# Performance work log

Measured on AMD Instinct MI355X. Metric: run time of the kernel, lower is better.

The kernel has to match this reference:

```python
import jax, jax.numpy as jnp
import numpy as np

B, ID, OD = 4096, 2048, 1024


def _conv_softmax(x, w):
    # x: [..., L]; torch Conv1d(1,1,k=3,stride=1,pad=1,bias=False) then softmax(dim=-1)
    L = x.shape[-1]
    xp = jnp.pad(x, [(0, 0)] * (x.ndim - 1) + [(1, 1)])
    y = w[0] * xp[..., 0:L] + w[1] * xp[..., 1:L + 1] + w[2] * xp[..., 2:L + 2]
    return jax.nn.softmax(y, axis=-1)


def _lstm_cell(x, h, c, Wih, Whh, bih, bhh):
    # torch LSTMCell gate order: i, f, g, o
    g = x @ Wih.T + h @ Whh.T + (bih + bhh)
    i, f, gg, o = jnp.split(g, 4, axis=-1)
    c2 = jax.nn.sigmoid(f) * c + jax.nn.sigmoid(i) * jnp.tanh(gg)
    h2 = jax.nn.sigmoid(o) * jnp.tanh(c2)
    return h2, c2


def _lstm_params(key, in_dim, hid):
    k = 1.0 / np.sqrt(hid)
    ks = jax.random.split(key, 4)
    Wih = jax.random.uniform(ks[0], (4 * hid, in_dim), jnp.float32, -k, k)
    Whh = jax.random.uniform(ks[1], (4 * hid, hid), jnp.float32, -k, k)
    bih = jax.random.uniform(ks[2], (4 * hid,), jnp.float32, -k, k)
    bhh = jax.random.uniform(ks[3], (4 * hid,), jnp.float32, -k, k)
    return Wih, Whh, bih, bhh


def setup_inputs() -> dict:
    key = jax.random.key(0)
    ks = jax.random.split(key, 12)
    spec = jax.random.normal(ks[0], (B, ID), jnp.float32)
    Wih1, Whh1, bih1, bhh1 = _lstm_params(ks[1], ID, OD)
    Wih2, Whh2, bih2, bhh2 = _lstm_params(ks[2], ID // 2, OD // 2)
    Wih3, Whh3, bih3, bhh3 = _lstm_params(ks[3], ID // 4, OD // 4)
    Wih4, Whh4, bih4, bhh4 = _lstm_params(ks[4], ID // 8, OD // 8)
    ck = np.sqrt(1.0 / 3.0)  # Conv1d(1,1,3) init bound
    w2_1h = jax.random.uniform(ks[5], (3,), jnp.float32, -ck, ck)
    w2_1c = jax.random.uniform(ks[6], (3,), jnp.float32, -ck, ck)
    w3_2h = jax.random.uniform(ks[7], (3,), jnp.float32, -ck, ck)
    w3_2c = jax.random.uniform(ks[8], (3,), jnp.float32, -ck, ck)
    w4_3h = jax.random.uniform(ks[9], (3,), jnp.float32, -ck, ck)
    w4_3c = jax.random.uniform(ks[10], (3,), jnp.float32, -ck, ck)
    return dict(spec=spec,
                Wih1=Wih1, Whh1=Whh1, bih1=bih1, bhh1=bhh1,
                Wih2=Wih2, Whh2=Whh2, bih2=bih2, bhh2=bhh2,
                Wih3=Wih3, Whh3=Whh3, bih3=bih3, bhh3=bhh3,
                Wih4=Wih4, Whh4=Whh4, bih4=bih4, bhh4=bhh4,
                w2_1h=w2_1h, w2_1c=w2_1c, w3_2h=w3_2h, w3_2c=w3_2c,
                w4_3h=w4_3h, w4_3c=w4_3c)


def reference(spec, Wih1, Whh1, bih1, bhh1, Wih2, Whh2, bih2, bhh2,
              Wih3, Whh3, bih3, bhh3, Wih4, Whh4, bih4, bhh4,
              w2_1h, w2_1c, w3_2h, w3_2c, w4_3h, w4_3c):
    b = spec.shape[0]
    # Level 4: 8 independent steps, fresh zero state each (torch code passes no hidden)
    x4 = spec.reshape(b, 8, ID // 8)
    z4 = jnp.zeros((b, 8, OD // 8), spec.dtype)
    h4, c4 = _lstm_cell(x4, z4, z4, Wih4, Whh4, bih4, bhh4)   # [b,8,OD/8]
    hb4 = _conv_softmax(h4.reshape(b, 4, OD // 4), w4_3h)      # pairs -> [b,4,OD/4]
    cb4 = _conv_softmax(c4.reshape(b, 4, OD // 4), w4_3c)
    # Level 3: 4 independent steps seeded by level-4 blended states
    x3 = spec.reshape(b, 4, ID // 4)
    h3, c3 = _lstm_cell(x3, hb4, cb4, Wih3, Whh3, bih3, bhh3)  # [b,4,OD/4]
    hb3 = _conv_softmax(h3.reshape(b, 2, OD // 2), w3_2h)      # [b,2,OD/2]
    cb3 = _conv_softmax(c3.reshape(b, 2, OD // 2), w3_2c)
    # Level 2: 2 independent steps
    x2 = spec.reshape(b, 2, ID // 2)
    h2, c2 = _lstm_cell(x2, hb3, cb3, Wih2, Whh2, bih2, bhh2)  # [b,2,OD/2]
    hb2 = _conv_softmax(h2.reshape(b, OD), w2_1h)              # [b,OD]
    cb2 = _conv_softmax(c2.reshape(b, OD), w2_1c)
    # Level 1: single full-resolution step; forward returns out1 = h1
    h1, c1 = _lstm_cell(spec, hb2, cb2, Wih1, Whh1, bih1, bhh1)
    return h1
```

## Files before the change

kernel.cpp:

```cpp
#include <hip/hip_runtime.h>


typedef __bf16 bf16x8 __attribute__((ext_vector_type(8)));
typedef float f32x4 __attribute__((ext_vector_type(4)));
typedef unsigned short u16x4 __attribute__((ext_vector_type(4)));
typedef unsigned short u16x8 __attribute__((ext_vector_type(8)));

#define AS1 __attribute__((address_space(1)))
#define AS3 __attribute__((address_space(3)))

__device__ __forceinline__ unsigned short f2bf(float f) {
    union { float f; unsigned int i; } v; v.f = f;
    unsigned int r = v.i + 0x7fffu + ((v.i >> 16) & 1u);
    return (unsigned short)(r >> 16);
}
__device__ __forceinline__ float bf2f(unsigned short u) {
    union { unsigned int i; float f; } v; v.i = ((unsigned int)u) << 16; return v.f;
}
__device__ __forceinline__ float sigm(float x) { return 1.f / (1.f + __expf(-x)); }
__device__ __forceinline__ float tanh_(float x) { float e = __expf(2.f * x); return 1.f - 2.f / (e + 1.f); }

struct PSeg { const float* src; unsigned short* dst; long g0; int H; int kshift; int dstld; int dstcol; };
struct PArgs {
    PSeg s[7];
    const float* spec; unsigned short* sB;
    const float *bi1, *bh1, *bi2, *bh2, *bi3, *bh3, *bi4, *bh4;
    float *bs1, *bs2, *bs3, *bs4;
};

__global__ __launch_bounds__(256) void prep_all(PArgs pa)
{
    const long NS = 2097152;
    const long NP = 4161536;
    const long total = NS + NP + 7680;
    const long stride = (long)gridDim.x * blockDim.x;
    for (long gi = (long)blockIdx.x * blockDim.x + threadIdx.x; gi < total; gi += stride) {
        if (gi < NS) {
            const float4 v = ((const float4*)pa.spec)[gi];
            u16x4 o; o.x = f2bf(v.x); o.y = f2bf(v.y); o.z = f2bf(v.z); o.w = f2bf(v.w);
            ((u16x4*)pa.sB)[gi] = o;
        } else if (gi < NS + NP) {
            const long gp = gi - NS;
            int si = 0;
#pragma unroll
            for (int k = 1; k < 7; ++k) si += (gp >= pa.s[k].g0);
            const PSeg sg = pa.s[si];
            const long i = gp - sg.g0;
            const int kq = 1 << sg.kshift;
            const int p = (int)(i >> sg.kshift);
            const int kk = ((int)i & (kq - 1)) << 2;
            const int o = ((p >> 6) << 4) | (p & 15);
            const int q = (p >> 4) & 3;
            const long r = (long)q * sg.H + o;
            const float4 v = *(const float4*)(sg.src + (r << (sg.kshift + 2)) + kk);
            u16x4 wv; wv.x = f2bf(v.x); wv.y = f2bf(v.y); wv.z = f2bf(v.z); wv.w = f2bf(v.w);
            *(u16x4*)(sg.dst + (long)p * sg.dstld + sg.dstcol + kk) = wv;
        } else {
            const int i = (int)(gi - NS - NP);
            const float *bih, *bhh; float* dst; int H, j;
            if (i < 4096)      { bih = pa.bi1; bhh = pa.bh1; dst = pa.bs1; H = 1024; j = i; }
            else if (i < 6144) { bih = pa.bi2; bhh = pa.bh2; dst = pa.bs2; H = 512;  j = i - 4096; }
            else if (i < 7168) { bih = pa.bi3; bhh = pa.bh3; dst = pa.bs3; H = 256;  j = i - 6144; }
            else               { bih = pa.bi4; bhh = pa.bh4; dst = pa.bs4; H = 128;  j = i - 7168; }
            const int o = ((j >> 6) << 4) | (j & 15);
            const int q = (j >> 4) & 3;
            dst[j] = bih[q * H + o] + bhh[q * H + o];
        }
    }
}

#define GLL(gsrc, loff) __builtin_amdgcn_global_load_lds(                                   \
    (const AS1 void*)(gsrc), (AS3 void*)(lds + (loff)), 16, 0, 0)

#define FENCE asm volatile("" ::: "memory")

#define STAGE_A(tts, qq)                                                                    \
    { if ((tts) < nk0) {                                                                    \
        const size_t ko = (size_t)(tts) * 64;                                               \
        GLL(A0 + a0off + ko,                   ((qq) << 15) + sd);                          \
        GLL(A0 + a0off + (size_t)32*K0 + ko,   ((qq) << 15) + 4096 + sd);                   \
        GLL(A0 + a0off + (size_t)64*K0 + ko,   ((qq) << 15) + 8192 + sd);                   \
        GLL(A0 + a0off + (size_t)96*K0 + ko,   ((qq) << 15) + 12288 + sd);                  \
    } else {                                                                                \
        const size_t ko = (size_t)((tts) - nk0) * 64;                                       \
        GLL(A1 + a1off + ko,                   ((qq) << 15) + sd);                          \
        GLL(A1 + a1off + (size_t)32*K1 + ko,   ((qq) << 15) + 4096 + sd);                   \
        GLL(A1 + a1off + (size_t)64*K1 + ko,   ((qq) << 15) + 8192 + sd);                   \
        GLL(A1 + a1off + (size_t)96*K1 + ko,   ((qq) << 15) + 12288 + sd);                  \
    } }

#define STAGE_B(tts, qq)                                                                    \
    { const size_t ko = (size_t)(tts) * 64;                                                 \
        GLL(W + boff + ko,                   ((qq) << 15) + 16384 + sd);                    \
        GLL(W + boff + (size_t)32*K + ko,    ((qq) << 15) + 20480 + sd);                    \
        GLL(W + boff + (size_t)64*K + ko,    ((qq) << 15) + 24576 + sd);                    \
        GLL(W + boff + (size_t)96*K + ko,    ((qq) << 15) + 28672 + sd); }

#define CLUSTER(MI, AF)                                                                     \
    { _Pragma("unroll") for (int mi = 0; mi < 2; ++mi) {                                    \
        _Pragma("unroll") for (int ni = 0; ni < 2; ++ni) {                                  \
            acc[(MI)+mi][ni] = __builtin_amdgcn_mfma_f32_16x16x32_bf16(                     \
                AF[mi][0], bF0[ni][0], acc[(MI)+mi][ni], 0, 0, 0);                          \
            acc[(MI)+mi][ni] = __builtin_amdgcn_mfma_f32_16x16x32_bf16(                     \
                AF[mi][1], bF0[ni][1], acc[(MI)+mi][ni], 0, 0, 0);                          \
            acc[(MI)+mi][ni+2] = __builtin_amdgcn_mfma_f32_16x16x32_bf16(                   \
                AF[mi][0], bF1[ni][0], acc[(MI)+mi][ni+2], 0, 0, 0);                        \
            acc[(MI)+mi][ni+2] = __builtin_amdgcn_mfma_f32_16x16x32_bf16(                   \
                AF[mi][1], bF1[ni][1], acc[(MI)+mi][ni+2], 0, 0, 0);                        \
    } } }

template<bool HAS_CIN, bool LAST>
__global__ __launch_bounds__(256, 2) void gemm8(
    const unsigned short* __restrict__ A0, const unsigned short* __restrict__ A1,
    const int K0, const int K1,
    const unsigned short* __restrict__ W,
    const float* __restrict__ bsum, const unsigned short* __restrict__ Cin,
    float* __restrict__ HoutF, unsigned short* __restrict__ HoutB,
    unsigned short* __restrict__ CoutB, const int H)
{
    __shared__ __align__(16) char lds[65536];
    const int t = threadIdx.x;
    const int w = t >> 6, l = t & 63;
    const int wr = w >> 1, wc = w & 1;
    const int K = K0 + K1;
    const int nk0 = K0 >> 6;

    const int GX = gridDim.x, GY = gridDim.y;
    const int nwg = GX * GY;
    const int bid = (int)blockIdx.y * GX + (int)blockIdx.x;
    const int swz = (bid & 7) * (nwg >> 3) + (bid >> 3);
    const int m0 = (swz / GY) * 128, n0 = (swz % GY) * 128;

    const int colsw = ((t & 7) ^ ((t >> 3) & 7)) * 8;
    const size_t a0off = (size_t)(m0 + (t >> 3)) * K0 + colsw;
    const size_t a1off = (size_t)(m0 + (t >> 3)) * K1 + colsw;
    const size_t boff  = (size_t)(n0 + (t >> 3)) * K  + colsw;
    const int sd = t * 16;

    const int lr128 = (l & 15) * 128;
    const int sw0 = (((l >> 4)    ) ^ (l & 7)) * 16;
    const int sw1 = (((l >> 4) + 4) ^ (l & 7)) * 16;

    f32x4 acc[4][4];
#pragma unroll
    for (int i = 0; i < 4; ++i)
#pragma unroll
        for (int j = 0; j < 4; ++j) acc[i][j] = (f32x4){0.f, 0.f, 0.f, 0.f};

    const int NT = K >> 6;

    STAGE_A(0, 0);
    STAGE_B(0, 0);
    STAGE_B(1, 1);

    bf16x8 aLo[2][2], aHi[2][2], bF0[2][2], bF1[2][2];

    for (int tt = 0; tt < NT; ++tt) {
        const int q = tt & 1, qn = q ^ 1;
        const int rbA = (q << 15) + wr * 8192 + lr128;
        const int rbB = (q << 15) + 16384 + wc * 8192 + lr128;
        const bool st1 = (tt + 1 < NT), st2 = (tt + 2 < NT);

        if (st1) { asm volatile("s_waitcnt vmcnt(4)" ::: "memory"); }
        else     { asm volatile("s_waitcnt vmcnt(0)" ::: "memory"); }
        __builtin_amdgcn_s_barrier();
        FENCE;

#pragma unroll
        for (int mi = 0; mi < 2; ++mi) {
            aLo[mi][0] = *(const bf16x8*)(lds + rbA + mi * 2048 + sw0);
            aLo[mi][1] = *(const bf16x8*)(lds + rbA + mi * 2048 + sw1);
        }
#pragma unroll
        for (int ni = 0; ni < 2; ++ni) {
            bF0[ni][0] = *(const bf16x8*)(lds + rbB + ni * 2048 + sw0);
            bF0[ni][1] = *(const bf16x8*)(lds + rbB + ni * 2048 + sw1);
            bF1[ni][0] = *(const bf16x8*)(lds + rbB + 4096 + ni * 2048 + sw0);
            bF1[ni][1] = *(const bf16x8*)(lds + rbB + 4096 + ni * 2048 + sw1);
        }
        if (st1) { STAGE_A(tt + 1, qn); }
#pragma unroll
        for (int mi = 0; mi < 2; ++mi) {
            aHi[mi][0] = *(const bf16x8*)(lds + rbA + 4096 + mi * 2048 + sw0);
            aHi[mi][1] = *(const bf16x8*)(lds + rbA + 4096 + mi * 2048 + sw1);
        }

        __builtin_amdgcn_s_setprio(1);
        CLUSTER(0, aLo);
        __builtin_amdgcn_s_setprio(0);
        __builtin_amdgcn_s_barrier();
        FENCE;

        if (st2) { STAGE_B(tt + 2, q); }
        __builtin_amdgcn_s_setprio(1);
        CLUSTER(2, aHi);
        __builtin_amdgcn_s_setprio(0);
    }

    const int ocol = (n0 >> 6) * 16 + wc * 16 + (l & 15);
    const int bb = n0 + wc * 64 + (l & 15);
    const float b0 = bsum[bb], b1 = bsum[bb + 16], b2 = bsum[bb + 32], b3 = bsum[bb + 48];
    const int mrow0 = m0 + wr * 64 + (l >> 4) * 4;
#pragma unroll
    for (int mi = 0; mi < 4; ++mi)
#pragma unroll
        for (int j = 0; j < 4; ++j) {
            const size_t m = (size_t)(mrow0 + mi * 16 + j);
            const float gi = acc[mi][0][j] + b0;
            const float gf = acc[mi][1][j] + b1;
            const float gg = acc[mi][2][j] + b2;
            const float go = acc[mi][3][j] + b3;
            float c2 = sigm(gi) * tanh_(gg);
            if (HAS_CIN) c2 += sigm(gf) * bf2f(Cin[m * H + ocol]);
            const float h2 = sigm(go) * tanh_(c2);
            if (LAST) {
                HoutF[m * H + ocol] = h2;
            } else {
                HoutB[m * H + ocol] = f2bf(h2);
                CoutB[m * H + ocol] = f2bf(c2);
            }
        }
}

template<int L>
__global__ __launch_bounds__(256) void conv_dual(
    const unsigned short* __restrict__ Hin, const unsigned short* __restrict__ Cin,
    const float* __restrict__ w3h, const float* __restrict__ w3c,
    unsigned short* __restrict__ hbuf, unsigned short* __restrict__ cbuf)
{
    constexpr int R = 2048 / L;
    constexpr int TPR = L / 8;
    __shared__ float xs[R][L + 2];
    __shared__ float red[8];
    const int nb = gridDim.x >> 1;
    const bool isC = (int)blockIdx.x >= nb;
    const int row0 = (isC ? (int)blockIdx.x - nb : (int)blockIdx.x) * R;
    const unsigned short* Xs = isC ? Cin : Hin;
    const float* w3 = isC ? w3c : w3h;
    const int t = threadIdx.x;
    const int r = t / TPR;
    const int c8 = (t % TPR) * 8;
    const float w0 = w3[0], w1 = w3[1], w2 = w3[2];

    const u16x8 v = *(const u16x8*)(Xs + (size_t)(row0 + r) * L + c8);
#pragma unroll
    for (int k = 0; k < 8; ++k) xs[r][c8 + 1 + k] = bf2f(v[k]);
    if (t < R) { xs[t][0] = 0.f; xs[t][L + 1] = 0.f; }
    __syncthreads();

    float y[8];
    float vmax = -3.4e38f;
#pragma unroll
    for (int k = 0; k < 8; ++k) {
        y[k] = w0 * xs[r][c8 + k] + w1 * xs[r][c8 + k + 1] + w2 * xs[r][c8 + k + 2];
        vmax = fmaxf(vmax, y[k]);
    }
#pragma unroll
    for (int off = (TPR >= 64 ? 32 : TPR / 2); off >= 1; off >>= 1)
        vmax = fmaxf(vmax, __shfl_xor(vmax, off));
    if (TPR == 128) {
        if ((t & 63) == 0) red[t >> 6] = vmax;
        __syncthreads();
        vmax = fmaxf(red[2 * r], red[2 * r + 1]);
    }
    float s = 0.f;
#pragma unroll
    for (int k = 0; k < 8; ++k) { y[k] = __expf(y[k] - vmax); s += y[k]; }
#pragma unroll
    for (int off = (TPR >= 64 ? 32 : TPR / 2); off >= 1; off >>= 1)
        s += __shfl_xor(s, off);
    if (TPR == 128) {
        if ((t & 63) == 0) red[4 + (t >> 6)] = s;
        __syncthreads();
        s = red[4 + 2 * r] + red[4 + 2 * r + 1];
    }
    const float inv = 1.f / s;
    u16x8 o;
#pragma unroll
    for (int k = 0; k < 8; ++k) o[k] = f2bf(y[k] * inv);
    if (isC) *(u16x8*)(cbuf + (size_t)(row0 + r) * L + c8) = o;
    else     *(u16x8*)(hbuf + (size_t)(row0 + r) * L + c8) = o;
}

extern "C" void kernel_launch(void* const* d_in, const int* in_sizes, int n_in,
                              void* d_out, int out_size, void* d_ws, size_t ws_size,
                              hipStream_t stream)
{
    (void)in_sizes; (void)n_in; (void)out_size; (void)ws_size;
    const float* spec  = (const float*)d_in[0];
    const float* Wih1  = (const float*)d_in[1];
    const float* Whh1  = (const float*)d_in[2];
    const float* bih1  = (const float*)d_in[3];
    const float* bhh1  = (const float*)d_in[4];
    const float* Wih2  = (const float*)d_in[5];
    const float* Whh2  = (const float*)d_in[6];
    const float* bih2  = (const float*)d_in[7];
    const float* bhh2  = (const float*)d_in[8];
    const float* Wih3  = (const float*)d_in[9];
    const float* Whh3  = (const float*)d_in[10];
    const float* bih3  = (const float*)d_in[11];
    const float* bhh3  = (const float*)d_in[12];
    const float* Wih4  = (const float*)d_in[13];
    const float* bih4  = (const float*)d_in[15];
    const float* bhh4  = (const float*)d_in[16];
    const float* w2_1h = (const float*)d_in[17];
    const float* w2_1c = (const float*)d_in[18];
    const float* w3_2h = (const float*)d_in[19];
    const float* w3_2c = (const float*)d_in[20];
    const float* w4_3h = (const float*)d_in[21];
    const float* w4_3c = (const float*)d_in[22];

    char* ws = (char*)d_ws;
    unsigned short* h   = (unsigned short*)(ws + 0);
    unsigned short* c   = (unsigned short*)(ws + (size_t)8388608);
    unsigned short* cb  = (unsigned short*)(ws + (size_t)16777216);
    unsigned short* hb  = (unsigned short*)(ws + (size_t)25165824);
    unsigned short* sB  = (unsigned short*)(ws + (size_t)33554432);
    unsigned short* Wc1 = (unsigned short*)(ws + (size_t)50331648);
    unsigned short* Wc2 = (unsigned short*)(ws + (size_t)75497472);
    unsigned short* Wc3 = (unsigned short*)(ws + (size_t)81788928);
    unsigned short* W4  = (unsigned short*)(ws + (size_t)83361792);
    float*          bs1 = (float*)(ws + (size_t)83623936);
    float*          bs2 = bs1 + 4096;
    float*          bs3 = bs2 + 4096;
    float*          bs4 = bs3 + 4096;

    PArgs pa;
    pa.s[0] = { Wih1, Wc1,       0, 1024, 9, 3072,    0 };
    pa.s[1] = { Whh1, Wc1, 2097152, 1024, 8, 3072, 2048 };
    pa.s[2] = { Wih2, Wc2, 3145728,  512, 8, 1536,    0 };
    pa.s[3] = { Whh2, Wc2, 3670016,  512, 7, 1536, 1024 };
    pa.s[4] = { Wih3, Wc3, 3932160,  256, 7,  768,    0 };
    pa.s[5] = { Whh3, Wc3, 4063232,  256, 6,  768,  512 };
    pa.s[6] = { Wih4, W4,  4128768,  128, 6,  256,    0 };
    pa.spec = spec; pa.sB = sB;
    pa.bi1 = bih1; pa.bh1 = bhh1; pa.bi2 = bih2; pa.bh2 = bhh2;
    pa.bi3 = bih3; pa.bh3 = bhh3; pa.bi4 = bih4; pa.bh4 = bhh4;
    pa.bs1 = bs1; pa.bs2 = bs2; pa.bs3 = bs3; pa.bs4 = bs4;
    prep_all<<<2048, 256, 0, stream>>>(pa);

    gemm8<false, false><<<dim3(256, 4), 256, 0, stream>>>(
        sB, nullptr, 256, 0, W4, bs4, nullptr, nullptr, h, c, 128);
    conv_dual<256><<<4096, 256, 0, stream>>>(h, c, w4_3h, w4_3c, hb, cb);

    gemm8<true, false><<<dim3(128, 8), 256, 0, stream>>>(
        sB, hb, 512, 256, Wc3, bs3, cb, nullptr, h, c, 256);
    conv_dual<512><<<4096, 256, 0, stream>>>(h, c, w3_2h, w3_2c, hb, cb);

    gemm8<true, false><<<dim3(64, 16), 256, 0, stream>>>(
        sB, hb, 1024, 512, Wc2, bs2, cb, nullptr, h, c, 512);
    conv_dual<1024><<<4096, 256, 0, stream>>>(h, c, w2_1h, w2_1c, hb, cb);

    gemm8<true, true><<<dim3(32, 32), 256, 0, stream>>>(
        sB, hb, 2048, 1024, Wc1, bs1, cb, (float*)d_out, nullptr, nullptr, 1024);
}
```

Before: 301.6 us.

## Enlarge GEMM workgroup tile to 256x256 with 16 waves

The fused LSTM-gate GEMM kernel moves from 128x128 tiles with 4 waves to 256x256 tiles with 16 waves per workgroup, arranged as a 4x4 wave grid. The LDS double buffer grows to 128KB and each thread now issues two global-to-LDS loads per operand per stage instead of four. Grids shrink by 4x, so the largest GEMM launches 256 workgroups instead of 1024. The aim is more operand reuse per global load and less redundant traffic, at the cost of one workgroup per CU, heavier barrier synchronisation, and reduced latency hiding.

New measurement: 522.8 us. 1.73x slower.

```diff
diff --git a/kernel.cpp b/kernel.cpp
--- a/kernel.cpp
+++ b/kernel.cpp
@@ -77,24 +77,18 @@
 #define STAGE_A(tts, qq)                                                                    \
     { if ((tts) < nk0) {                                                                    \
         const size_t ko = (size_t)(tts) * 64;                                               \
-        GLL(A0 + a0off + ko,                   ((qq) << 15) + sd);                          \
-        GLL(A0 + a0off + (size_t)32*K0 + ko,   ((qq) << 15) + 4096 + sd);                   \
-        GLL(A0 + a0off + (size_t)64*K0 + ko,   ((qq) << 15) + 8192 + sd);                   \
-        GLL(A0 + a0off + (size_t)96*K0 + ko,   ((qq) << 15) + 12288 + sd);                  \
+        GLL(A0 + a0off0 + ko, ((qq) << 16) + sd);                                           \
+        GLL(A0 + a0off1 + ko, ((qq) << 16) + 16384 + sd);                                   \
     } else {                                                                                \
         const size_t ko = (size_t)((tts) - nk0) * 64;                                       \
-        GLL(A1 + a1off + ko,                   ((qq) << 15) + sd);                          \
-        GLL(A1 + a1off + (size_t)32*K1 + ko,   ((qq) << 15) + 4096 + sd);                   \
-        GLL(A1 + a1off + (size_t)64*K1 + ko,   ((qq) << 15) + 8192 + sd);                   \
-        GLL(A1 + a1off + (size_t)96*K1 + ko,   ((qq) << 15) + 12288 + sd);                  \
+        GLL(A1 + a1off0 + ko, ((qq) << 16) + sd);                                           \
+        GLL(A1 + a1off1 + ko, ((qq) << 16) + 16384 + sd);                                   \
     } }
 
 #define STAGE_B(tts, qq)                                                                    \
     { const size_t ko = (size_t)(tts) * 64;                                                 \
-        GLL(W + boff + ko,                   ((qq) << 15) + 16384 + sd);                    \
-        GLL(W + boff + (size_t)32*K + ko,    ((qq) << 15) + 20480 + sd);                    \
-        GLL(W + boff + (size_t)64*K + ko,    ((qq) << 15) + 24576 + sd);                    \
-        GLL(W + boff + (size_t)96*K + ko,    ((qq) << 15) + 28672 + sd); }
+        GLL(W + boff0 + ko, ((qq) << 16) + 32768 + sd);                                     \
+        GLL(W + boff1 + ko, ((qq) << 16) + 49152 + sd); }
 
 #define CLUSTER(MI, AF)                                                                     \
     { _Pragma("unroll") for (int mi = 0; mi < 2; ++mi) {                                    \
@@ -110,7 +104,7 @@
     } } }
 
 template<bool HAS_CIN, bool LAST>
-__global__ __launch_bounds__(256, 2) void gemm8(
+__global__ __launch_bounds__(1024, 1) void gemm16(
     const unsigned short* __restrict__ A0, const unsigned short* __restrict__ A1,
     const int K0, const int K1,
     const unsigned short* __restrict__ W,
@@ -118,10 +112,10 @@
     float* __restrict__ HoutF, unsigned short* __restrict__ HoutB,
     unsigned short* __restrict__ CoutB, const int H)
 {
-    __shared__ __align__(16) char lds[65536];
+    __shared__ __align__(16) char lds[131072];
     const int t = threadIdx.x;
     const int w = t >> 6, l = t & 63;
-    const int wr = w >> 1, wc = w & 1;
+    const int wr = w >> 2, wc = w & 3;
     const int K = K0 + K1;
     const int nk0 = K0 >> 6;
 
@@ -129,12 +123,16 @@
     const int nwg = GX * GY;
     const int bid = (int)blockIdx.y * GX + (int)blockIdx.x;
     const int swz = (bid & 7) * (nwg >> 3) + (bid >> 3);
-    const int m0 = (swz / GY) * 128, n0 = (swz % GY) * 128;
+    const int m0 = (swz / GY) * 256, n0 = (swz % GY) * 256;
 
     const int colsw = ((t & 7) ^ ((t >> 3) & 7)) * 8;
-    const size_t a0off = (size_t)(m0 + (t >> 3)) * K0 + colsw;
-    const size_t a1off = (size_t)(m0 + (t >> 3)) * K1 + colsw;
-    const size_t boff  = (size_t)(n0 + (t >> 3)) * K  + colsw;
+    const int arow = m0 + (t >> 3);
+    const size_t a0off0 = (size_t)arow * K0 + colsw;
+    const size_t a0off1 = a0off0 + (size_t)128 * K0;
+    const size_t a1off0 = (size_t)arow * K1 + colsw;
+    const size_t a1off1 = a1off0 + (size_t)128 * K1;
+    const size_t boff0 = (size_t)(n0 + (t >> 3)) * K + colsw;
+    const size_t boff1 = boff0 + (size_t)128 * K;
     const int sd = t * 16;
 
     const int lr128 = (l & 15) * 128;
@@ -157,11 +155,11 @@
 
     for (int tt = 0; tt < NT; ++tt) {
         const int q = tt & 1, qn = q ^ 1;
-        const int rbA = (q << 15) + wr * 8192 + lr128;
-        const int rbB = (q << 15) + 16384 + wc * 8192 + lr128;
+        const int rbA = (q << 16) + wr * 8192 + lr128;
+        const int rbB = (q << 16) + 32768 + wc * 8192 + lr128;
         const bool st1 = (tt + 1 < NT), st2 = (tt + 2 < NT);
 
-        if (st1) { asm volatile("s_waitcnt vmcnt(4)" ::: "memory"); }
+        if (st1) { asm volatile("s_waitcnt vmcnt(2)" ::: "memory"); }
         else     { asm volatile("s_waitcnt vmcnt(0)" ::: "memory"); }
         __builtin_amdgcn_s_barrier();
         FENCE;
@@ -339,18 +337,18 @@
     pa.bs1 = bs1; pa.bs2 = bs2; pa.bs3 = bs3; pa.bs4 = bs4;
     prep_all<<<2048, 256, 0, stream>>>(pa);
 
-    gemm8<false, false><<<dim3(256, 4), 256, 0, stream>>>(
+    gemm16<false, false><<<dim3(128, 2), 1024, 0, stream>>>(
         sB, nullptr, 256, 0, W4, bs4, nullptr, nullptr, h, c, 128);
     conv_dual<256><<<4096, 256, 0, stream>>>(h, c, w4_3h, w4_3c, hb, cb);
 
-    gemm8<true, false><<<dim3(128, 8), 256, 0, stream>>>(
+    gemm16<true, false><<<dim3(64, 4), 1024, 0, stream>>>(
         sB, hb, 512, 256, Wc3, bs3, cb, nullptr, h, c, 256);
     conv_dual<512><<<4096, 256, 0, stream>>>(h, c, w3_2h, w3_2c, hb, cb);
 
-    gemm8<true, false><<<dim3(64, 16), 256, 0, stream>>>(
+    gemm16<true, false><<<dim3(32, 8), 1024, 0, stream>>>(
         sB, hb, 1024, 512, Wc2, bs2, cb, nullptr, h, c, 512);
     conv_dual<1024><<<4096, 256, 0, stream>>>(h, c, w2_1h, w2_1c, hb, cb);
 
-    gemm8<true, true><<<dim3(32, 32), 256, 0, stream>>>(
+    gemm16<true, true><<<dim3(16, 16), 1024, 0, stream>>>(
         sB, hb, 2048, 1024, Wc1, bs1, cb, (float*)d_out, nullptr, nullptr, 1024);
 }
```
